# Kernel optimization log

Hardware: AMD Instinct MI355X
Metric: run time of the kernel (lower is better)

## Reference

```python
import jax, jax.numpy as jnp
import numpy as np

H = 2048
D = 66
T = 4096

def _lstm_cell(x, h, c, W_ih, W_hh, b_ih, b_hh):
    # x: [1, in], h/c: [1, H]; torch LSTMCell gate order: i, f, g, o
    gates = x @ W_ih.T + h @ W_hh.T + b_ih + b_hh  # [1, 4H]
    i, f, g, o = jnp.split(gates, 4, axis=-1)
    i = jax.nn.sigmoid(i)
    f = jax.nn.sigmoid(f)
    g = jnp.tanh(g)
    o = jax.nn.sigmoid(o)
    c_new = f * c + i * g
    h_new = o * jnp.tanh(c_new)
    return h_new, c_new

def setup_inputs() -> dict:
    key = jax.random.key(0)
    ks = jax.random.split(key, 12)
    s1 = 1.0 / np.sqrt(H)
    mk = lambda k, shp: jax.random.uniform(k, shp, jnp.float32, -s1, s1)
    return {
        "y": jax.random.normal(ks[0], (T, D), jnp.float32),
        "W_ih1": mk(ks[1], (4 * H, D)),
        "W_hh1": mk(ks[2], (4 * H, H)),
        "b_ih1": mk(ks[3], (4 * H,)),
        "b_hh1": mk(ks[4], (4 * H,)),
        "W_ih2": mk(ks[5], (4 * H, H)),
        "W_hh2": mk(ks[6], (4 * H, H)),
        "b_ih2": mk(ks[7], (4 * H,)),
        "b_hh2": mk(ks[8], (4 * H,)),
        "W_lin": mk(ks[9], (D, H)),
        "b_lin": mk(ks[10], (D,)),
        "pre_output_len": 64,
    }

def reference(y, W_ih1, W_hh1, b_ih1, b_hh1, W_ih2, W_hh2, b_ih2, b_hh2, W_lin, b_lin, pre_output_len):
    frames = y[:, None, :]  # [T, 1, D]

    def step(carry, x):
        h1, c1, h2, c2 = carry
        h1, c1 = _lstm_cell(x, h1, c1, W_ih1, W_hh1, b_ih1, b_hh1)
        h2, c2 = _lstm_cell(h1, h2, c2, W_ih2, W_hh2, b_ih2, b_hh2)
        out = h2 @ W_lin.T + b_lin  # [1, D]
        return (h1, c1, h2, c2), out

    z = jnp.zeros((1, H), jnp.float32)
    _, outs = jax.lax.scan(step, (z, z, z, z), frames)  # [T, 1, D]
    return outs[pre_output_len:]
```

## Files before the change

### kernel.cpp

```cpp
#include <hip/hip_runtime.h>
#include <math.h>

#define HH 2048
#define DD 66
#define TT 4096
#define PRE 64
#define NWG 256
#define RPW 8
#define FSTRIDE 16


__device__ __forceinline__ float sigmoidf_(float x) {
  return 1.0f / (1.0f + expf(-x));
}

__device__ __forceinline__ void gbar_wait(unsigned* flags, unsigned target, int tid) {
  unsigned v = __hip_atomic_load(&flags[tid * FSTRIDE], __ATOMIC_RELAXED, __HIP_MEMORY_SCOPE_AGENT);
  while (!__syncthreads_and((int)(v == target))) {
    v = __hip_atomic_load(&flags[tid * FSTRIDE], __ATOMIC_RELAXED, __HIP_MEMORY_SCOPE_AGENT);
  }
}

__global__ __launch_bounds__(256, 1) void lstm_persist(
    const float* __restrict__ y,
    const float* __restrict__ Wih1, const float* __restrict__ Whh1,
    const float* __restrict__ bih1, const float* __restrict__ bhh1,
    const float* __restrict__ Wih2, const float* __restrict__ Whh2,
    const float* __restrict__ bih2, const float* __restrict__ bhh2,
    const float* __restrict__ Wlin, const float* __restrict__ blin,
    float* __restrict__ out,
    float* h1buf, float* h2buf, unsigned* flags1, unsigned* flags2)
{
  __shared__ __align__(16) float ldsH1[HH];
  __shared__ __align__(16) float ldsH2[HH];
  __shared__ float ldsX[DD];
  __shared__ float g1s[4][RPW];
  __shared__ float g2s[4][RPW];
  __shared__ float c1s[RPW];
  __shared__ float c2s[RPW];
  __shared__ float red[4];

  const int tid  = threadIdx.x;
  const int wg   = blockIdx.x;
  const int wave = tid >> 6;
  const int lane = tid & 63;
  const int rowbase = wg * RPW;
  const int grow0   = wave * HH + rowbase;

  for (int i = tid; i < HH; i += 256) { ldsH1[i] = 0.0f; ldsH2[i] = 0.0f; }
  if (tid < RPW) {
    c1s[tid] = 0.0f; c2s[tid] = 0.0f;
    __hip_atomic_store(&h2buf[HH + rowbase + tid], 0.0f, __ATOMIC_RELAXED, __HIP_MEMORY_SCOPE_AGENT);
  }
  __syncthreads();

  for (int t = 0; t < TT; ++t) {
    if (tid < DD) ldsX[tid] = y[t * DD + tid];
    __syncthreads();

    {
      float4 acc[RPW];
      #pragma unroll
      for (int r = 0; r < RPW; ++r) acc[r] = make_float4(0.f, 0.f, 0.f, 0.f);
      const float4* h4 = (const float4*)ldsH1;
      #pragma unroll 2
      for (int j = 0; j < 8; ++j) {
        const float4 hv = h4[j * 64 + lane];
        #pragma unroll
        for (int r = 0; r < RPW; ++r) {
          const float4* Wr = (const float4*)(Whh1 + (size_t)(grow0 + r) * HH);
          float4 wv = Wr[j * 64 + lane];
          acc[r].x = fmaf(wv.x, hv.x, acc[r].x);
          acc[r].y = fmaf(wv.y, hv.y, acc[r].y);
          acc[r].z = fmaf(wv.z, hv.z, acc[r].z);
          acc[r].w = fmaf(wv.w, hv.w, acc[r].w);
        }
      }
      #pragma unroll
      for (int r = 0; r < RPW; ++r) {
        const int grow = grow0 + r;
        float a = (acc[r].x + acc[r].y) + (acc[r].z + acc[r].w);
        const float* Xr = Wih1 + (size_t)grow * DD;
        a += Xr[lane] * ldsX[lane];
        if (lane < DD - 64) a += Xr[64 + lane] * ldsX[64 + lane];
        #pragma unroll
        for (int s = 32; s > 0; s >>= 1) a += __shfl_xor(a, s, 64);
        if (lane == 0) g1s[wave][r] = a + bih1[grow] + bhh1[grow];
      }
    }
    __syncthreads();

    if (tid < RPW) {
      float gi = sigmoidf_(g1s[0][tid]);
      float gf = sigmoidf_(g1s[1][tid]);
      float gg = tanhf(g1s[2][tid]);
      float go = sigmoidf_(g1s[3][tid]);
      float c  = fmaf(gf, c1s[tid], gi * gg);
      c1s[tid] = c;
      float h  = go * tanhf(c);
      __hip_atomic_store(&h1buf[(t & 1) * HH + rowbase + tid], h,
                         __ATOMIC_RELAXED, __HIP_MEMORY_SCOPE_AGENT);
    }
    __syncthreads();
    if (tid == 0)
      __hip_atomic_store(&flags1[wg * FSTRIDE], (unsigned)(t + 1),
                         __ATOMIC_RELEASE, __HIP_MEMORY_SCOPE_AGENT);
    gbar_wait(flags1, (unsigned)(t + 1), tid);

    for (int i = tid; i < HH; i += 256) {
      ldsH1[i] = __hip_atomic_load(&h1buf[(t & 1) * HH + i],
                                   __ATOMIC_RELAXED, __HIP_MEMORY_SCOPE_AGENT);
      ldsH2[i] = __hip_atomic_load(&h2buf[((t + 1) & 1) * HH + i],
                                   __ATOMIC_RELAXED, __HIP_MEMORY_SCOPE_AGENT);
    }
    __syncthreads();

    {
      float4 acc[RPW];
      #pragma unroll
      for (int r = 0; r < RPW; ++r) acc[r] = make_float4(0.f, 0.f, 0.f, 0.f);
      const float4* ha = (const float4*)ldsH1;
      const float4* hb = (const float4*)ldsH2;
      #pragma unroll 2
      for (int j = 0; j < 8; ++j) {
        const float4 va = ha[j * 64 + lane];
        const float4 vb = hb[j * 64 + lane];
        #pragma unroll
        for (int r = 0; r < RPW; ++r) {
          const float4* Wa = (const float4*)(Wih2 + (size_t)(grow0 + r) * HH);
          const float4* Wb = (const float4*)(Whh2 + (size_t)(grow0 + r) * HH);
          float4 wa = Wa[j * 64 + lane];
          float4 wb = Wb[j * 64 + lane];
          acc[r].x = fmaf(wa.x, va.x, acc[r].x);
          acc[r].y = fmaf(wa.y, va.y, acc[r].y);
          acc[r].z = fmaf(wa.z, va.z, acc[r].z);
          acc[r].w = fmaf(wa.w, va.w, acc[r].w);
          acc[r].x = fmaf(wb.x, vb.x, acc[r].x);
          acc[r].y = fmaf(wb.y, vb.y, acc[r].y);
          acc[r].z = fmaf(wb.z, vb.z, acc[r].z);
          acc[r].w = fmaf(wb.w, vb.w, acc[r].w);
        }
      }
      #pragma unroll
      for (int r = 0; r < RPW; ++r) {
        const int grow = grow0 + r;
        float a = (acc[r].x + acc[r].y) + (acc[r].z + acc[r].w);
        #pragma unroll
        for (int s = 32; s > 0; s >>= 1) a += __shfl_xor(a, s, 64);
        if (lane == 0) g2s[wave][r] = a + bih2[grow] + bhh2[grow];
      }
    }
    __syncthreads();

    if (tid < RPW) {
      float gi = sigmoidf_(g2s[0][tid]);
      float gf = sigmoidf_(g2s[1][tid]);
      float gg = tanhf(g2s[2][tid]);
      float go = sigmoidf_(g2s[3][tid]);
      float c  = fmaf(gf, c2s[tid], gi * gg);
      c2s[tid] = c;
      float h  = go * tanhf(c);
      __hip_atomic_store(&h2buf[(t & 1) * HH + rowbase + tid], h,
                         __ATOMIC_RELAXED, __HIP_MEMORY_SCOPE_AGENT);
    }
    __syncthreads();
    if (tid == 0)
      __hip_atomic_store(&flags2[wg * FSTRIDE], (unsigned)(t + 1),
                         __ATOMIC_RELEASE, __HIP_MEMORY_SCOPE_AGENT);

    if (wg < DD && t >= PRE + 1) {
      const float4* Wr = (const float4*)(Wlin + (size_t)wg * HH);
      const float4* h4 = (const float4*)ldsH2;
      float p = 0.f;
      #pragma unroll
      for (int j = 0; j < 2; ++j) {
        int idx = tid + j * 256;
        float4 wv = Wr[idx]; float4 hv = h4[idx];
        p += wv.x * hv.x + wv.y * hv.y + wv.z * hv.z + wv.w * hv.w;
      }
      #pragma unroll
      for (int s = 32; s > 0; s >>= 1) p += __shfl_xor(p, s, 64);
      if (lane == 0) red[wave] = p;
      __syncthreads();
      if (tid == 0)
        out[(size_t)(t - 1 - PRE) * DD + wg] = red[0] + red[1] + red[2] + red[3] + blin[wg];
    }

    gbar_wait(flags2, (unsigned)(t + 1), tid);
  }

  if (wg < DD) {
    for (int i = tid; i < HH; i += 256)
      ldsH2[i] = __hip_atomic_load(&h2buf[((TT - 1) & 1) * HH + i],
                                   __ATOMIC_RELAXED, __HIP_MEMORY_SCOPE_AGENT);
    __syncthreads();
    const float4* Wr = (const float4*)(Wlin + (size_t)wg * HH);
    const float4* h4 = (const float4*)ldsH2;
    float p = 0.f;
    #pragma unroll
    for (int j = 0; j < 2; ++j) {
      int idx = tid + j * 256;
      float4 wv = Wr[idx]; float4 hv = h4[idx];
      p += wv.x * hv.x + wv.y * hv.y + wv.z * hv.z + wv.w * hv.w;
    }
    #pragma unroll
    for (int s = 32; s > 0; s >>= 1) p += __shfl_xor(p, s, 64);
    if (lane == 0) red[wave] = p;
    __syncthreads();
    if (tid == 0)
      out[(size_t)(TT - 1 - PRE) * DD + wg] = red[0] + red[1] + red[2] + red[3] + blin[wg];
  }
}

extern "C" void kernel_launch(void* const* d_in, const int* in_sizes, int n_in,
                              void* d_out, int out_size, void* d_ws, size_t ws_size,
                              hipStream_t stream) {
  const float* y    = (const float*)d_in[0];
  const float* Wih1 = (const float*)d_in[1];
  const float* Whh1 = (const float*)d_in[2];
  const float* bih1 = (const float*)d_in[3];
  const float* bhh1 = (const float*)d_in[4];
  const float* Wih2 = (const float*)d_in[5];
  const float* Whh2 = (const float*)d_in[6];
  const float* bih2 = (const float*)d_in[7];
  const float* bhh2 = (const float*)d_in[8];
  const float* Wlin = (const float*)d_in[9];
  const float* blin = (const float*)d_in[10];
  float* out = (float*)d_out;

  char* ws = (char*)d_ws;
  float*    h1buf  = (float*)(ws);
  float*    h2buf  = (float*)(ws + 2 * HH * sizeof(float));
  unsigned* flags1 = (unsigned*)(ws + 4 * HH * sizeof(float));
  unsigned* flags2 = flags1 + NWG * FSTRIDE;

  void* args[] = { &y, &Wih1, &Whh1, &bih1, &bhh1, &Wih2, &Whh2, &bih2, &bhh2,
                   &Wlin, &blin, &out, &h1buf, &h2buf, &flags1, &flags2 };
  hipLaunchCooperativeKernel((const void*)lstm_persist, dim3(NWG), dim3(256),
                             args, 0, stream);
}
```

Baseline: 199.4 ms.

## Quantize recurrent weights to int16 per-row and double threads per workgroup

Adds a pre-pass that packs W_hh1, W_ih2 and W_hh2 into per-row scaled int16, so the persistent kernel streams half as many weight bytes each timestep and dequantizes inline. The persistent kernel goes from 256 to 512 threads, with two waves per gate, and loads h into registers once per step. Biases and scales are cached in LDS. Lower weight precision may change numerics, and the quantized path only runs when the workspace is large enough.

```diff
diff --git a/kernel.cpp b/kernel.cpp
--- a/kernel.cpp
+++ b/kernel.cpp
@@ -6,22 +6,82 @@
 #define TT 4096
 #define PRE 64
 #define NWG 256
-#define RPW 8
+#define NTH 512
 #define FSTRIDE 16
 
 
-__device__ __forceinline__ float sigmoidf_(float x) {
-  return 1.0f / (1.0f + expf(-x));
+typedef unsigned int uint;
+
+__device__ __forceinline__ float sigmoidf_(float x) { return 1.0f / (1.0f + expf(-x)); }
+
+__device__ __forceinline__ float wred(float a) {
+  #pragma unroll
+  for (int s = 32; s > 0; s >>= 1) a += __shfl_xor(a, s, 64);
+  return a;
 }
 
 __device__ __forceinline__ void gbar_wait(unsigned* flags, unsigned target, int tid) {
-  unsigned v = __hip_atomic_load(&flags[tid * FSTRIDE], __ATOMIC_RELAXED, __HIP_MEMORY_SCOPE_AGENT);
+  const int idx = (tid & (NWG - 1)) * FSTRIDE;
+  unsigned v = __hip_atomic_load(&flags[idx], __ATOMIC_RELAXED, __HIP_MEMORY_SCOPE_AGENT);
   while (!__syncthreads_and((int)(v == target))) {
-    v = __hip_atomic_load(&flags[tid * FSTRIDE], __ATOMIC_RELAXED, __HIP_MEMORY_SCOPE_AGENT);
-  }
-}
-
-__global__ __launch_bounds__(256, 1) void lstm_persist(
+    v = __hip_atomic_load(&flags[idx], __ATOMIC_RELAXED, __HIP_MEMORY_SCOPE_AGENT);
+  }
+}
+
+__device__ __forceinline__ float dqdot(uint4 q, float4 ha, float4 hb, float acc) {
+  acc = fmaf((float)((int)(short)(q.x & 0xffffu)), ha.x, acc);
+  acc = fmaf((float)(((int)q.x) >> 16),            ha.y, acc);
+  acc = fmaf((float)((int)(short)(q.y & 0xffffu)), ha.z, acc);
+  acc = fmaf((float)(((int)q.y) >> 16),            ha.w, acc);
+  acc = fmaf((float)((int)(short)(q.z & 0xffffu)), hb.x, acc);
+  acc = fmaf((float)(((int)q.z) >> 16),            hb.y, acc);
+  acc = fmaf((float)((int)(short)(q.w & 0xffffu)), hb.z, acc);
+  acc = fmaf((float)(((int)q.w) >> 16),            hb.w, acc);
+  return acc;
+}
+
+__global__ void pack_q16(const float* __restrict__ src, uint4* __restrict__ q,
+                         float* __restrict__ scale) {
+  __shared__ float rmx[256];
+  __shared__ float sinv_s;
+  const int row = blockIdx.x;
+  const int tid = threadIdx.x;
+  const int p = tid >> 6, lane = tid & 63;
+  const float* sr = src + (size_t)row * HH + p * 512 + 4 * lane;
+  float4 a = *(const float4*)sr;
+  float4 b = *(const float4*)(sr + 256);
+  float m = fmaxf(fmaxf(fmaxf(fabsf(a.x), fabsf(a.y)), fmaxf(fabsf(a.z), fabsf(a.w))),
+                  fmaxf(fmaxf(fabsf(b.x), fabsf(b.y)), fmaxf(fabsf(b.z), fabsf(b.w))));
+  rmx[tid] = m;
+  __syncthreads();
+  for (int s = 128; s > 0; s >>= 1) {
+    if (tid < s) rmx[tid] = fmaxf(rmx[tid], rmx[tid + s]);
+    __syncthreads();
+  }
+  if (tid == 0) {
+    float rm = rmx[0];
+    sinv_s = rm > 0.f ? 32767.f / rm : 0.f;
+    scale[row] = rm > 0.f ? rm / 32767.f : 0.f;
+  }
+  __syncthreads();
+  const float inv = sinv_s;
+  float w[8] = {a.x, a.y, a.z, a.w, b.x, b.y, b.z, b.w};
+  int qi[8];
+  #pragma unroll
+  for (int j = 0; j < 8; ++j) {
+    int v = __float2int_rn(w[j] * inv);
+    qi[j] = max(-32767, min(32767, v));
+  }
+  uint4 out;
+  out.x = ((uint)qi[0] & 0xffffu) | ((uint)qi[1] << 16);
+  out.y = ((uint)qi[2] & 0xffffu) | ((uint)qi[3] << 16);
+  out.z = ((uint)qi[4] & 0xffffu) | ((uint)qi[5] << 16);
+  out.w = ((uint)qi[6] & 0xffffu) | ((uint)qi[7] << 16);
+  q[((size_t)row * 4 + p) * 64 + lane] = out;
+}
+
+template <bool QUANT>
+__global__ __launch_bounds__(NTH, 1) void lstm_persist(
     const float* __restrict__ y,
     const float* __restrict__ Wih1, const float* __restrict__ Whh1,
     const float* __restrict__ bih1, const float* __restrict__ bhh1,
@@ -29,26 +89,43 @@
     const float* __restrict__ bih2, const float* __restrict__ bhh2,
     const float* __restrict__ Wlin, const float* __restrict__ blin,
     float* __restrict__ out,
+    const uint4* __restrict__ Q1, const float* __restrict__ S1,
+    const uint4* __restrict__ Q2a, const float* __restrict__ S2a,
+    const uint4* __restrict__ Q2b, const float* __restrict__ S2b,
     float* h1buf, float* h2buf, unsigned* flags1, unsigned* flags2)
 {
   __shared__ __align__(16) float ldsH1[HH];
   __shared__ __align__(16) float ldsH2[HH];
   __shared__ float ldsX[DD];
-  __shared__ float g1s[4][RPW];
-  __shared__ float g2s[4][RPW];
-  __shared__ float c1s[RPW];
-  __shared__ float c2s[RPW];
-  __shared__ float red[4];
-
-  const int tid  = threadIdx.x;
-  const int wg   = blockIdx.x;
+  __shared__ float g1s[4][8];
+  __shared__ float g2s[4][8];
+  __shared__ float c1s[8];
+  __shared__ float c2s[8];
+  __shared__ float red[8];
+  __shared__ float bsum1[32], bsum2[32];
+  __shared__ float s1r[32], sAr[32], sBr[32];
+
+  const int tid = threadIdx.x;
+  const int wg = blockIdx.x;
   const int wave = tid >> 6;
   const int lane = tid & 63;
-  const int rowbase = wg * RPW;
-  const int grow0   = wave * HH + rowbase;
-
-  for (int i = tid; i < HH; i += 256) { ldsH1[i] = 0.0f; ldsH2[i] = 0.0f; }
-  if (tid < RPW) {
+  const int gate = wave >> 1;
+  const int half = wave & 1;
+  const int rowbase = wg * 8;
+
+  for (int i = tid; i < HH; i += NTH) { ldsH1[i] = 0.0f; ldsH2[i] = 0.0f; }
+  if (tid < 32) {
+    int g = tid >> 3, sr2 = tid & 7;
+    int grow = g * HH + rowbase + sr2;
+    bsum1[tid] = bih1[grow] + bhh1[grow];
+    bsum2[tid] = bih2[grow] + bhh2[grow];
+    if constexpr (QUANT) {
+      s1r[tid] = S1[grow];
+      sAr[tid] = S2a[grow];
+      sBr[tid] = S2b[grow];
+    }
+  }
+  if (tid < 8) {
     c1s[tid] = 0.0f; c2s[tid] = 0.0f;
     __hip_atomic_store(&h2buf[HH + rowbase + tid], 0.0f, __ATOMIC_RELAXED, __HIP_MEMORY_SCOPE_AGENT);
   }
@@ -59,45 +136,51 @@
     __syncthreads();
 
     {
-      float4 acc[RPW];
-      #pragma unroll
-      for (int r = 0; r < RPW; ++r) acc[r] = make_float4(0.f, 0.f, 0.f, 0.f);
-      const float4* h4 = (const float4*)ldsH1;
-      #pragma unroll 2
-      for (int j = 0; j < 8; ++j) {
-        const float4 hv = h4[j * 64 + lane];
-        #pragma unroll
-        for (int r = 0; r < RPW; ++r) {
-          const float4* Wr = (const float4*)(Whh1 + (size_t)(grow0 + r) * HH);
-          float4 wv = Wr[j * 64 + lane];
-          acc[r].x = fmaf(wv.x, hv.x, acc[r].x);
-          acc[r].y = fmaf(wv.y, hv.y, acc[r].y);
-          acc[r].z = fmaf(wv.z, hv.z, acc[r].z);
-          acc[r].w = fmaf(wv.w, hv.w, acc[r].w);
+      float4 hf[8];
+      const float4* H4 = (const float4*)ldsH1;
+      #pragma unroll
+      for (int m = 0; m < 8; ++m) hf[m] = H4[m * 64 + lane];
+
+      #pragma unroll
+      for (int r = 0; r < 4; ++r) {
+        const int srow = half * 4 + r;
+        const int grow = gate * HH + rowbase + srow;
+        float v;
+        if constexpr (QUANT) {
+          const uint4* Qp = Q1 + ((size_t)grow * 4) * 64 + lane;
+          float acc = 0.f;
+          #pragma unroll
+          for (int p = 0; p < 4; ++p)
+            acc = dqdot(Qp[p * 64], hf[2 * p], hf[2 * p + 1], acc);
+          v = acc * s1r[gate * 8 + srow];
+        } else {
+          const float4* Wr = (const float4*)(Whh1 + (size_t)grow * HH) + lane;
+          float acc = 0.f;
+          #pragma unroll
+          for (int m = 0; m < 8; ++m) {
+            const float4 wv = Wr[m * 64];
+            acc = fmaf(wv.x, hf[m].x, acc); acc = fmaf(wv.y, hf[m].y, acc);
+            acc = fmaf(wv.z, hf[m].z, acc); acc = fmaf(wv.w, hf[m].w, acc);
+          }
+          v = acc;
         }
+        const float* Xr = Wih1 + (size_t)grow * DD;
+        v += Xr[lane] * ldsX[lane];
+        if (lane < DD - 64) v += Xr[64 + lane] * ldsX[64 + lane];
+        v = wred(v);
+        if (lane == 0) g1s[gate][srow] = v + bsum1[gate * 8 + srow];
       }
-      #pragma unroll
-      for (int r = 0; r < RPW; ++r) {
-        const int grow = grow0 + r;
-        float a = (acc[r].x + acc[r].y) + (acc[r].z + acc[r].w);
-        const float* Xr = Wih1 + (size_t)grow * DD;
-        a += Xr[lane] * ldsX[lane];
-        if (lane < DD - 64) a += Xr[64 + lane] * ldsX[64 + lane];
-        #pragma unroll
-        for (int s = 32; s > 0; s >>= 1) a += __shfl_xor(a, s, 64);
-        if (lane == 0) g1s[wave][r] = a + bih1[grow] + bhh1[grow];
-      }
-    }
-    __syncthreads();
-
-    if (tid < RPW) {
+    }
+    __syncthreads();
+
+    if (tid < 8) {
       float gi = sigmoidf_(g1s[0][tid]);
       float gf = sigmoidf_(g1s[1][tid]);
       float gg = tanhf(g1s[2][tid]);
       float go = sigmoidf_(g1s[3][tid]);
-      float c  = fmaf(gf, c1s[tid], gi * gg);
+      float c = fmaf(gf, c1s[tid], gi * gg);
       c1s[tid] = c;
-      float h  = go * tanhf(c);
+      float h = go * tanhf(c);
       __hip_atomic_store(&h1buf[(t & 1) * HH + rowbase + tid], h,
                          __ATOMIC_RELAXED, __HIP_MEMORY_SCOPE_AGENT);
     }
@@ -107,7 +190,7 @@
                          __ATOMIC_RELEASE, __HIP_MEMORY_SCOPE_AGENT);
     gbar_wait(flags1, (unsigned)(t + 1), tid);
 
-    for (int i = tid; i < HH; i += 256) {
+    for (int i = tid; i < HH; i += NTH) {
       ldsH1[i] = __hip_atomic_load(&h1buf[(t & 1) * HH + i],
                                    __ATOMIC_RELAXED, __HIP_MEMORY_SCOPE_AGENT);
       ldsH2[i] = __hip_atomic_load(&h2buf[((t + 1) & 1) * HH + i],
@@ -116,50 +199,55 @@
     __syncthreads();
 
     {
-      float4 acc[RPW];
-      #pragma unroll
-      for (int r = 0; r < RPW; ++r) acc[r] = make_float4(0.f, 0.f, 0.f, 0.f);
-      const float4* ha = (const float4*)ldsH1;
-      const float4* hb = (const float4*)ldsH2;
-      #pragma unroll 2
-      for (int j = 0; j < 8; ++j) {
-        const float4 va = ha[j * 64 + lane];
-        const float4 vb = hb[j * 64 + lane];
-        #pragma unroll
-        for (int r = 0; r < RPW; ++r) {
-          const float4* Wa = (const float4*)(Wih2 + (size_t)(grow0 + r) * HH);
-          const float4* Wb = (const float4*)(Whh2 + (size_t)(grow0 + r) * HH);
-          float4 wa = Wa[j * 64 + lane];
-          float4 wb = Wb[j * 64 + lane];
-          acc[r].x = fmaf(wa.x, va.x, acc[r].x);
-          acc[r].y = fmaf(wa.y, va.y, acc[r].y);
-          acc[r].z = fmaf(wa.z, va.z, acc[r].z);
-          acc[r].w = fmaf(wa.w, va.w, acc[r].w);
-          acc[r].x = fmaf(wb.x, vb.x, acc[r].x);
-          acc[r].y = fmaf(wb.y, vb.y, acc[r].y);
-          acc[r].z = fmaf(wb.z, vb.z, acc[r].z);
-          acc[r].w = fmaf(wb.w, vb.w, acc[r].w);
+      float4 hf1[8], hf2[8];
+      const float4* Ha = (const float4*)ldsH1;
+      const float4* Hb = (const float4*)ldsH2;
+      #pragma unroll
+      for (int m = 0; m < 8; ++m) { hf1[m] = Ha[m * 64 + lane]; hf2[m] = Hb[m * 64 + lane]; }
+
+      #pragma unroll
+      for (int r = 0; r < 4; ++r) {
+        const int srow = half * 4 + r;
+        const int grow = gate * HH + rowbase + srow;
+        float v;
+        if constexpr (QUANT) {
+          const uint4* Qa = Q2a + ((size_t)grow * 4) * 64 + lane;
+          const uint4* Qb = Q2b + ((size_t)grow * 4) * 64 + lane;
+          float aa = 0.f, ab = 0.f;
+          #pragma unroll
+          for (int p = 0; p < 4; ++p) {
+            aa = dqdot(Qa[p * 64], hf1[2 * p], hf1[2 * p + 1], aa);
+            ab = dqdot(Qb[p * 64], hf2[2 * p], hf2[2 * p + 1], ab);
+          }
+          v = aa * sAr[gate * 8 + srow] + ab * sBr[gate * 8 + srow];
+        } else {
+          const float4* Wa = (const float4*)(Wih2 + (size_t)grow * HH) + lane;
+          const float4* Wb = (const float4*)(Whh2 + (size_t)grow * HH) + lane;
+          float acc = 0.f;
+          #pragma unroll
+          for (int m = 0; m < 8; ++m) {
+            const float4 a2 = Wa[m * 64], b2 = Wb[m * 64];
+            acc = fmaf(a2.x, hf1[m].x, acc); acc = fmaf(a2.y, hf1[m].y, acc);
+            acc = fmaf(a2.z, hf1[m].z, acc); acc = fmaf(a2.w, hf1[m].w, acc);
+            acc = fmaf(b2.x, hf2[m].x, acc); acc = fmaf(b2.y, hf2[m].y, acc);
+            acc = fmaf(b2.z, hf2[m].z, acc); acc = fmaf(b2.w, hf2[m].w, acc);
+          }
+          v = acc;
         }
+        v = wred(v);
+        if (lane == 0) g2s[gate][srow] = v + bsum2[gate * 8 + srow];
       }
-      #pragma unroll
-      for (int r = 0; r < RPW; ++r) {
-        const int grow = grow0 + r;
-        float a = (acc[r].x + acc[r].y) + (acc[r].z + acc[r].w);
-        #pragma unroll
-        for (int s = 32; s > 0; s >>= 1) a += __shfl_xor(a, s, 64);
-        if (lane == 0) g2s[wave][r] = a + bih2[grow] + bhh2[grow];
-      }
-    }
-    __syncthreads();
-
-    if (tid < RPW) {
+    }
+    __syncthreads();
+
+    if (tid < 8) {
       float gi = sigmoidf_(g2s[0][tid]);
       float gf = sigmoidf_(g2s[1][tid]);
       float gg = tanhf(g2s[2][tid]);
       float go = sigmoidf_(g2s[3][tid]);
-      float c  = fmaf(gf, c2s[tid], gi * gg);
+      float c = fmaf(gf, c2s[tid], gi * gg);
       c2s[tid] = c;
-      float h  = go * tanhf(c);
+      float h = go * tanhf(c);
       __hip_atomic_store(&h2buf[(t & 1) * HH + rowbase + tid], h,
                          __ATOMIC_RELAXED, __HIP_MEMORY_SCOPE_AGENT);
     }
@@ -171,44 +259,40 @@
     if (wg < DD && t >= PRE + 1) {
       const float4* Wr = (const float4*)(Wlin + (size_t)wg * HH);
       const float4* h4 = (const float4*)ldsH2;
-      float p = 0.f;
-      #pragma unroll
-      for (int j = 0; j < 2; ++j) {
-        int idx = tid + j * 256;
-        float4 wv = Wr[idx]; float4 hv = h4[idx];
-        p += wv.x * hv.x + wv.y * hv.y + wv.z * hv.z + wv.w * hv.w;
-      }
-      #pragma unroll
-      for (int s = 32; s > 0; s >>= 1) p += __shfl_xor(p, s, 64);
+      float4 wv = Wr[tid]; float4 hv = h4[tid];
+      float p = wv.x * hv.x + wv.y * hv.y + wv.z * hv.z + wv.w * hv.w;
+      p = wred(p);
       if (lane == 0) red[wave] = p;
       __syncthreads();
-      if (tid == 0)
-        out[(size_t)(t - 1 - PRE) * DD + wg] = red[0] + red[1] + red[2] + red[3] + blin[wg];
+      if (tid == 0) {
+        float o = blin[wg];
+        #pragma unroll
+        for (int w = 0; w < 8; ++w) o += red[w];
+        out[(size_t)(t - 1 - PRE) * DD + wg] = o;
+      }
     }
 
     gbar_wait(flags2, (unsigned)(t + 1), tid);
   }
 
   if (wg < DD) {
-    for (int i = tid; i < HH; i += 256)
+    for (int i = tid; i < HH; i += NTH)
       ldsH2[i] = __hip_atomic_load(&h2buf[((TT - 1) & 1) * HH + i],
                                    __ATOMIC_RELAXED, __HIP_MEMORY_SCOPE_AGENT);
     __syncthreads();
     const float4* Wr = (const float4*)(Wlin + (size_t)wg * HH);
     const float4* h4 = (const float4*)ldsH2;
-    float p = 0.f;
-    #pragma unroll
-    for (int j = 0; j < 2; ++j) {
-      int idx = tid + j * 256;
-      float4 wv = Wr[idx]; float4 hv = h4[idx];
-      p += wv.x * hv.x + wv.y * hv.y + wv.z * hv.z + wv.w * hv.w;
-    }
-    #pragma unroll
-    for (int s = 32; s > 0; s >>= 1) p += __shfl_xor(p, s, 64);
+    float4 wv = Wr[tid]; float4 hv = h4[tid];
+    float p = wv.x * hv.x + wv.y * hv.y + wv.z * hv.z + wv.w * hv.w;
+    p = wred(p);
     if (lane == 0) red[wave] = p;
     __syncthreads();
-    if (tid == 0)
-      out[(size_t)(TT - 1 - PRE) * DD + wg] = red[0] + red[1] + red[2] + red[3] + blin[wg];
+    if (tid == 0) {
+      float o = blin[wg];
+      #pragma unroll
+      for (int w = 0; w < 8; ++w) o += red[w];
+      out[(size_t)(TT - 1 - PRE) * DD + wg] = o;
+    }
   }
 }
 
@@ -229,13 +313,39 @@
   float* out = (float*)d_out;
 
   char* ws = (char*)d_ws;
-  float*    h1buf  = (float*)(ws);
-  float*    h2buf  = (float*)(ws + 2 * HH * sizeof(float));
-  unsigned* flags1 = (unsigned*)(ws + 4 * HH * sizeof(float));
+  const size_t qB = (size_t)4 * HH * HH * 2;
+  const size_t sB = (size_t)4 * HH * 4;
+  const size_t per = qB + sB;
+  const size_t tail_bytes = (size_t)4 * HH * sizeof(float) + (size_t)2 * NWG * FSTRIDE * 4;
+  const bool quant = ws_size >= 3 * per + tail_bytes;
+
+  const uint4 *Q1 = nullptr, *Q2a = nullptr, *Q2b = nullptr;
+  const float *S1 = nullptr, *S2a = nullptr, *S2b = nullptr;
+  char* tail = ws;
+  if (quant) {
+    uint4* q1 = (uint4*)ws;              float* s1 = (float*)(ws + qB);
+    uint4* q2 = (uint4*)(ws + per);      float* s2 = (float*)(ws + per + qB);
+    uint4* q3 = (uint4*)(ws + 2 * per);  float* s3 = (float*)(ws + 2 * per + qB);
+    tail = ws + 3 * per;
+    pack_q16<<<4 * HH, 256, 0, stream>>>(Whh1, q1, s1);
+    pack_q16<<<4 * HH, 256, 0, stream>>>(Wih2, q2, s2);
+    pack_q16<<<4 * HH, 256, 0, stream>>>(Whh2, q3, s3);
+    Q1 = q1; S1 = s1; Q2a = q2; S2a = s2; Q2b = q3; S2b = s3;
+  }
+  float* h1buf = (float*)tail;
+  float* h2buf = h1buf + 2 * HH;
+  unsigned* flags1 = (unsigned*)(h2buf + 2 * HH);
   unsigned* flags2 = flags1 + NWG * FSTRIDE;
 
   void* args[] = { &y, &Wih1, &Whh1, &bih1, &bhh1, &Wih2, &Whh2, &bih2, &bhh2,
-                   &Wlin, &blin, &out, &h1buf, &h2buf, &flags1, &flags2 };
-  hipLaunchCooperativeKernel((const void*)lstm_persist, dim3(NWG), dim3(256),
-                             args, 0, stream);
-}
+                   &Wlin, &blin, &out,
+                   &Q1, &S1, &Q2a, &S2a, &Q2b, &S2b,
+                   &h1buf, &h2buf, &flags1, &flags2 };
+  if (quant) {
+    hipLaunchCooperativeKernel(reinterpret_cast<const void*>(lstm_persist<true>),
+                               dim3(NWG), dim3(NTH), args, 0, stream);
+  } else {
+    hipLaunchCooperativeKernel(reinterpret_cast<const void*>(lstm_persist<false>),
+                               dim3(NWG), dim3(NTH), args, 0, stream);
+  }
+}
```

Measured after the change: 340.8 ms. 71.0% more time.
